# Kernel optimization log

Hardware: AMD Instinct MI355X
Metric: run time of the kernel (lower is better)

Reference implementation:

```python
import jax, jax.numpy as jnp
import numpy as np

B, S, D, F, K = 32, 512, 256, 256, 3

def setup_inputs() -> dict:
    key = jax.random.key(0)
    ks = jax.random.split(key, 8)
    x = jax.random.normal(ks[0], (B, S, D), dtype=jnp.float32)
    target = jax.random.uniform(ks[1], (B, S), dtype=jnp.float32, minval=1.0, maxval=8.0)
    expand_max_len = int(jnp.round(target.sum(-1)).max())
    sc = 0.05
    conv1_w = jax.random.normal(ks[2], (F, D, K), dtype=jnp.float32) * sc
    conv1_b = jnp.zeros((F,), jnp.float32)
    conv2_w = jax.random.normal(ks[3], (F, F, K), dtype=jnp.float32) * sc
    conv2_b = jnp.zeros((F,), jnp.float32)
    norm1_g = jnp.ones((F,), jnp.float32); norm1_b = jnp.zeros((F,), jnp.float32)
    norm2_g = jnp.ones((F,), jnp.float32); norm2_b = jnp.zeros((F,), jnp.float32)
    lin_w = jax.random.normal(ks[4], (F,), dtype=jnp.float32) * sc
    lin_b = jnp.zeros((), jnp.float32)
    return {"x": x, "target": target, "conv1_w": conv1_w, "conv1_b": conv1_b,
            "conv2_w": conv2_w, "conv2_b": conv2_b, "norm1_g": norm1_g, "norm1_b": norm1_b,
            "norm2_g": norm2_g, "norm2_b": norm2_b, "lin_w": lin_w, "lin_b": lin_b,
            "expand_max_len": expand_max_len}

def _layernorm(h, g, b, eps=1e-5):
    mu = jnp.mean(h, axis=-1, keepdims=True)
    var = jnp.mean((h - mu) ** 2, axis=-1, keepdims=True)
    return (h - mu) * jax.lax.rsqrt(var + eps) * g + b

def _conv1d(h_bsd, w, bias):
    # h_bsd: [B,S,C] -> conv over time with 'same' padding -> [B,S,F]
    h = jnp.transpose(h_bsd, (0, 2, 1))  # [B,C,S]
    out = jax.lax.conv_general_dilated(h, w, window_strides=(1,),
                                       padding=[(K // 2, K // 2)],
                                       dimension_numbers=("NCH", "OIH", "NCH"))
    out = out + bias[None, :, None]
    return jnp.transpose(out, (0, 2, 1))  # [B,S,F]

def _duration_predict(x, conv1_w, conv1_b, conv2_w, conv2_b,
                      norm1_g, norm1_b, norm2_g, norm2_b, lin_w, lin_b):
    h = _conv1d(x, conv1_w, conv1_b)
    h = jax.nn.relu(_layernorm(h, norm1_g, norm1_b))  # dropout is identity in eval
    h = _conv1d(h, conv2_w, conv2_b)
    h = jax.nn.relu(_layernorm(h, norm2_g, norm2_b))
    return jax.nn.relu(h @ lin_w + lin_b)  # [B,S]

def _length_regulate(x, target, L):
    d = jnp.round(target)                # [B,S] integer-valued durations
    ends = jnp.cumsum(d, axis=-1)        # [B,S]
    starts = ends - d
    t = jnp.arange(L, dtype=d.dtype)     # [L]
    mask = ((t[None, None, :] >= starts[:, :, None]) &
            (t[None, None, :] < ends[:, :, None])).astype(x.dtype)  # [B,S,L]
    # x^T @ mask -> [B,D,L]; return transposed [B,L,D]
    return jnp.einsum("bsd,bsl->bld", x, mask)

def reference(x, target, conv1_w, conv1_b, conv2_w, conv2_b,
              norm1_g, norm1_b, norm2_g, norm2_b, lin_w, lin_b, expand_max_len):
    predicted_len = _duration_predict(x, conv1_w, conv1_b, conv2_w, conv2_b,
                                      norm1_g, norm1_b, norm2_g, norm2_b, lin_w, lin_b)
    output = _length_regulate(x, target, expand_max_len)
    return (output, predicted_len)
```

## Files before the change

kernel.cpp:

```cpp
#include <hip/hip_runtime.h>
#include <hip/hip_bf16.h>

#define NB 32
#define NS 512
#define NC 256
#define NKSTEP 24
#define ROWS 32
#define HALO_ROWS 34

typedef __attribute__((ext_vector_type(8))) short short8;
typedef __attribute__((ext_vector_type(4))) float f32x4;

__device__ __forceinline__ unsigned pack2(float a, float b) {
    __hip_bfloat16 ha = __float2bfloat16(a), hb = __float2bfloat16(b);
    return ((unsigned)(*(unsigned short*)&hb) << 16) | (unsigned)(*(unsigned short*)&ha);
}

__global__ __launch_bounds__(256) void prep_w2(const float* __restrict__ w1,
                                               const float* __restrict__ w2,
                                               unsigned short* __restrict__ Bp1,
                                               unsigned short* __restrict__ Bp2) {
    const bool second = blockIdx.x >= 256;
    const int f = blockIdx.x & 255, t = threadIdx.x;
    const float* w = second ? w2 : w1;
    unsigned short* Bp = second ? Bp2 : Bp1;
    const float* wf = w + (size_t)f * 768 + t * 3;
    const float v[3] = {wf[0], wf[1], wf[2]};
#pragma unroll
    for (int shift = 0; shift < 3; ++shift) {
        const int k = shift * 256 + t;
        const int o = f * 32 + (k >> 5) * 8192 + (k & 31);
        __hip_bfloat16 h = __float2bfloat16(v[shift]);
        Bp[o] = *(unsigned short*)&h;
    }
}

template <bool FINAL, typename Tin>
__global__ __launch_bounds__(256, 2) void conv_mfma(
    const Tin* __restrict__ in,
    const uint4* __restrict__ Bp,
    const float* __restrict__ bias,
    const float* __restrict__ gamma,
    const float* __restrict__ beta,
    const float* __restrict__ linw,
    const float* __restrict__ linb,
    void* __restrict__ outp)
{
    __shared__ __align__(16) uint4 xs[HALO_ROWS * 32];
    __shared__ float red[ROWS][4][2];
    __shared__ float dotb[ROWS][4];

    const int tid = threadIdx.x;
    const int b   = blockIdx.x >> 4;
    const int s0  = (blockIdx.x & 15) << 5;

    {
        const int slot = tid & 31;
        for (int r = tid >> 5; r < HALO_ROWS; r += 8) {
            const int s = s0 - 1 + r;
            uint4 v = {0u, 0u, 0u, 0u};
            if (s >= 0 && s < NS) {
                if constexpr (sizeof(Tin) == 4) {
                    const float* src = (const float*)in + ((size_t)(b * NS + s)) * NC + slot * 8;
                    const float4 lo = *(const float4*)src;
                    const float4 hi = *(const float4*)(src + 4);
                    v.x = pack2(lo.x, lo.y); v.y = pack2(lo.z, lo.w);
                    v.z = pack2(hi.x, hi.y); v.w = pack2(hi.z, hi.w);
                } else {
                    v = *(const uint4*)((const unsigned short*)in +
                                        ((size_t)(b * NS + s)) * NC + slot * 8);
                }
            }
            xs[r * 32 + (slot ^ ((r & 7) << 2))] = v;
        }
    }
    __syncthreads();

    const int lane = tid & 63;
    const int w    = tid >> 6;
    const int n0   = w << 6;
    const int l15  = lane & 15;
    const int lg   = lane >> 4;

    f32x4 acc[2][4];
#pragma unroll
    for (int mi = 0; mi < 2; ++mi)
#pragma unroll
        for (int ni = 0; ni < 4; ++ni) acc[mi][ni] = (f32x4){0.f, 0.f, 0.f, 0.f};

    const uint4* bbase = Bp + (size_t)(n0 + l15) * 4 + lg;

    auto lda = [&](int ks, int mi) -> short8 {
        const int row  = mi * 16 + l15 + (ks >> 3);
        int slot = ((ks & 7) << 2) + lg;
        slot ^= (row & 7) << 2;
        return *(const short8*)&xs[row * 32 + slot];
    };
    auto ldb = [&](int ks, int ni) -> short8 {
        return *(const short8*)(const void*)(bbase + ks * 1024 + ni * 64);
    };

    short8 areg[2][2], breg[4][4];
#pragma unroll
    for (int q = 0; q < 4; ++q)
#pragma unroll
        for (int ni = 0; ni < 4; ++ni) breg[q][ni] = ldb(q, ni);
#pragma unroll
    for (int p = 0; p < 2; ++p)
#pragma unroll
        for (int mi = 0; mi < 2; ++mi) areg[p][mi] = lda(p, mi);

#pragma unroll
    for (int p = 0; p < NKSTEP; ++p) {
        const int bs = p & 3, as = p & 1;
#pragma unroll
        for (int mi = 0; mi < 2; ++mi)
#pragma unroll
            for (int ni = 0; ni < 4; ++ni)
                acc[mi][ni] = __builtin_amdgcn_mfma_f32_16x16x32_bf16(
                    areg[as][mi], breg[bs][ni], acc[mi][ni], 0, 0, 0);
        if (p + 4 < NKSTEP) {
#pragma unroll
            for (int ni = 0; ni < 4; ++ni) breg[bs][ni] = ldb(p + 4, ni);
        }
        if (p + 2 < NKSTEP) {
#pragma unroll
            for (int mi = 0; mi < 2; ++mi) areg[as][mi] = lda(p + 2, mi);
        }
    }

    float bv[4], gv[4], bt[4], lwv[4];
#pragma unroll
    for (int ni = 0; ni < 4; ++ni) {
        const int col = n0 + ni * 16 + l15;
        bv[ni] = bias[col]; gv[ni] = gamma[col]; bt[ni] = beta[col];
        if constexpr (FINAL) lwv[ni] = linw[col];
    }
#pragma unroll
    for (int mi = 0; mi < 2; ++mi)
#pragma unroll
        for (int ni = 0; ni < 4; ++ni)
#pragma unroll
            for (int i = 0; i < 4; ++i) acc[mi][ni][i] += bv[ni];

#pragma unroll
    for (int mi = 0; mi < 2; ++mi) {
        float s[4] = {0, 0, 0, 0}, q[4] = {0, 0, 0, 0};
#pragma unroll
        for (int ni = 0; ni < 4; ++ni)
#pragma unroll
            for (int i = 0; i < 4; ++i) {
                const float v = acc[mi][ni][i];
                s[i] += v; q[i] += v * v;
            }
#pragma unroll
        for (int i = 0; i < 4; ++i)
#pragma unroll
            for (int m = 1; m < 16; m <<= 1) {
                s[i] += __shfl_xor(s[i], m, 64);
                q[i] += __shfl_xor(q[i], m, 64);
            }
        if (l15 == 0) {
#pragma unroll
            for (int i = 0; i < 4; ++i) {
                red[mi * 16 + lg * 4 + i][w][0] = s[i];
                red[mi * 16 + lg * 4 + i][w][1] = q[i];
            }
        }
    }
    __syncthreads();

#pragma unroll
    for (int mi = 0; mi < 2; ++mi) {
#pragma unroll
        for (int i = 0; i < 4; ++i) {
            const int row = mi * 16 + lg * 4 + i;
            float sum = 0.f, sq = 0.f;
#pragma unroll
            for (int ww = 0; ww < 4; ++ww) { sum += red[row][ww][0]; sq += red[row][ww][1]; }
            const float mu = sum * (1.f / 256.f);
            const float rs = rsqrtf(sq * (1.f / 256.f) - mu * mu + 1e-5f);
            float p = 0.f;
#pragma unroll
            for (int ni = 0; ni < 4; ++ni) {
                const float y = fmaxf(0.f, (acc[mi][ni][i] - mu) * rs * gv[ni] + bt[ni]);
                if constexpr (!FINAL) {
                    __hip_bfloat16 h = __float2bfloat16(y);
                    ((unsigned short*)outp)[((size_t)(b * NS + s0 + row)) * NC +
                                            n0 + ni * 16 + l15] = *(unsigned short*)&h;
                } else {
                    p += y * lwv[ni];
                }
            }
            if constexpr (FINAL) {
#pragma unroll
                for (int m = 1; m < 16; m <<= 1) p += __shfl_xor(p, m, 64);
                if (l15 == 0) dotb[row][w] = p;
            }
        }
    }
    if constexpr (FINAL) {
        __syncthreads();
        if (tid < ROWS) {
            const float tot = dotb[tid][0] + dotb[tid][1] + dotb[tid][2] + dotb[tid][3] + linb[0];
            ((float*)outp)[b * NS + s0 + tid] = fmaxf(0.f, tot);
        }
    }
}

__global__ __launch_bounds__(256) void scan_scatter(const float* __restrict__ target,
                                                    int* __restrict__ idx, int L)
{
    __shared__ int bufa[512], bufb[512];
    const int b = blockIdx.x, t = threadIdx.x;
    const float* tb = target + (size_t)b * NS;
    const int d0 = (int)rintf(tb[t]);
    const int d1 = (int)rintf(tb[t + 256]);
    bufa[t] = d0; bufa[t + 256] = d1;
    __syncthreads();
    int* src = bufa;
    int* dst = bufb;
    for (int off = 1; off < 512; off <<= 1) {
        for (int i = t; i < 512; i += 256) {
            int v = src[i];
            if (i >= off) v += src[i - off];
            dst[i] = v;
        }
        __syncthreads();
        int* tmp = src; src = dst; dst = tmp;
    }
    const int e0 = src[t], e1 = src[t + 256], total = src[511];
    int* ib = idx + (size_t)b * L;
    for (int k = e0 - d0; k < e0; ++k) ib[k] = t;
    for (int k = e1 - d1; k < e1; ++k) ib[k] = t + 256;
    for (int k = total + t; k < L; k += 256) ib[k] = -1;
}

__global__ __launch_bounds__(256) void gather2(const float4* __restrict__ x4,
                                               const int* __restrict__ idx,
                                               float4* __restrict__ out4, int L)
{
    const int b     = blockIdx.y;
    const int frame = blockIdx.x * 4 + (threadIdx.x >> 6);
    const int lane  = threadIdx.x & 63;
    if (frame >= L) return;
    const int pos = idx[(size_t)b * L + frame];
    float4 v = {0.f, 0.f, 0.f, 0.f};
    if (pos >= 0) v = x4[(((size_t)(b * NS + pos)) << 6) + lane];
    out4[(((size_t)b * L + frame) << 6) + lane] = v;
}

extern "C" void kernel_launch(void* const* d_in, const int* in_sizes, int n_in,
                              void* d_out, int out_size, void* d_ws, size_t ws_size,
                              hipStream_t stream)
{
    const float* x    = (const float*)d_in[0];
    const float* targ = (const float*)d_in[1];
    const float* c1w  = (const float*)d_in[2];
    const float* c1b  = (const float*)d_in[3];
    const float* c2w  = (const float*)d_in[4];
    const float* c2b  = (const float*)d_in[5];
    const float* n1g  = (const float*)d_in[6];
    const float* n1b  = (const float*)d_in[7];
    const float* n2g  = (const float*)d_in[8];
    const float* n2b  = (const float*)d_in[9];
    const float* lw   = (const float*)d_in[10];
    const float* lb   = (const float*)d_in[11];

    const int L = (out_size - NB * NS) / (NB * NC);

    unsigned short* Bp1 = (unsigned short*)d_ws;
    unsigned short* Bp2 = Bp1 + 196608;
    unsigned short* h1  = Bp2 + 196608;
    int* idx = (int*)(h1 + (size_t)NB * NS * NC);
    float* out  = (float*)d_out;
    float* pred = out + (size_t)NB * (size_t)L * NC;

    prep_w2<<<dim3(512), 256, 0, stream>>>(c1w, c2w, Bp1, Bp2);

    conv_mfma<false, float><<<dim3(NB * 16), 256, 0, stream>>>(
        x, (const uint4*)Bp1, c1b, n1g, n1b, nullptr, nullptr, (void*)h1);
    conv_mfma<true, unsigned short><<<dim3(NB * 16), 256, 0, stream>>>(
        h1, (const uint4*)Bp2, c2b, n2g, n2b, lw, lb, (void*)pred);

    scan_scatter<<<dim3(NB), 256, 0, stream>>>(targ, idx, L);
    gather2<<<dim3((L + 3) / 4, NB), 256, 0, stream>>>(
        (const float4*)x, idx, (float4*)out, L);
}
```

Baseline: 162.0 us.

## Merge weight prep with duration scan and tune conv prefetch and gather

```diff
diff --git a/kernel.cpp b/kernel.cpp
--- a/kernel.cpp
+++ b/kernel.cpp
@@ -16,27 +16,59 @@
     return ((unsigned)(*(unsigned short*)&hb) << 16) | (unsigned)(*(unsigned short*)&ha);
 }
 
-__global__ __launch_bounds__(256) void prep_w2(const float* __restrict__ w1,
-                                               const float* __restrict__ w2,
-                                               unsigned short* __restrict__ Bp1,
-                                               unsigned short* __restrict__ Bp2) {
-    const bool second = blockIdx.x >= 256;
-    const int f = blockIdx.x & 255, t = threadIdx.x;
-    const float* w = second ? w2 : w1;
-    unsigned short* Bp = second ? Bp2 : Bp1;
-    const float* wf = w + (size_t)f * 768 + t * 3;
-    const float v[3] = {wf[0], wf[1], wf[2]};
-#pragma unroll
-    for (int shift = 0; shift < 3; ++shift) {
-        const int k = shift * 256 + t;
-        const int o = f * 32 + (k >> 5) * 8192 + (k & 31);
-        __hip_bfloat16 h = __float2bfloat16(v[shift]);
-        Bp[o] = *(unsigned short*)&h;
-    }
+__global__ __launch_bounds__(256) void prep_and_scan(
+    const float* __restrict__ w1, const float* __restrict__ w2,
+    unsigned short* __restrict__ Bp1, unsigned short* __restrict__ Bp2,
+    const float* __restrict__ target, int* __restrict__ idx, int L)
+{
+    __shared__ int bufa[512], bufb[512];
+    const int t = threadIdx.x;
+
+    if (blockIdx.x < 512) {
+        const bool second = blockIdx.x >= 256;
+        const int f = blockIdx.x & 255;
+        const float* w = second ? w2 : w1;
+        unsigned short* Bp = second ? Bp2 : Bp1;
+        const float* wf = w + (size_t)f * 768 + t * 3;
+        const float v[3] = {wf[0], wf[1], wf[2]};
+#pragma unroll
+        for (int shift = 0; shift < 3; ++shift) {
+            const int k = shift * 256 + t;
+            const int o = f * 32 + (k >> 5) * 8192 + (k & 31);
+            __hip_bfloat16 h = __float2bfloat16(v[shift]);
+            Bp[o] = *(unsigned short*)&h;
+        }
+        return;
+    }
+
+    const int b = blockIdx.x - 512;
+    const float* tb = target + (size_t)b * NS;
+    const int d0 = (int)rintf(tb[t]);
+    const int d1 = (int)rintf(tb[t + 256]);
+    bufa[t] = d0; bufa[t + 256] = d1;
+    __syncthreads();
+    int* src = bufa;
+    int* dst = bufb;
+    for (int off = 1; off < 512; off <<= 1) {
+        for (int i = t; i < 512; i += 256) {
+            int v = src[i];
+            if (i >= off) v += src[i - off];
+            dst[i] = v;
+        }
+        __syncthreads();
+        int* tmp = src; src = dst; dst = tmp;
+    }
+    const int e0 = src[t], e1 = src[t + 256], total = src[511];
+    int* ib = idx + (size_t)b * L;
+    const int hi0 = e0 < L ? e0 : L;
+    const int hi1 = e1 < L ? e1 : L;
+    for (int k = e0 - d0; k < hi0; ++k) ib[k] = t;
+    for (int k = e1 - d1; k < hi1; ++k) ib[k] = t + 256;
+    for (int k = total + t; k < L; k += 256) ib[k] = -1;
 }
 
 template <bool FINAL, typename Tin>
-__global__ __launch_bounds__(256, 2) void conv_mfma(
+__global__ __launch_bounds__(256, 4) void conv_mfma(
     const Tin* __restrict__ in,
     const uint4* __restrict__ Bp,
     const float* __restrict__ bias,
@@ -100,32 +132,29 @@
         return *(const short8*)(const void*)(bbase + ks * 1024 + ni * 64);
     };
 
-    short8 areg[2][2], breg[4][4];
-#pragma unroll
-    for (int q = 0; q < 4; ++q)
+    short8 areg[2][2], breg[2][4];
+#pragma unroll
+    for (int q = 0; q < 2; ++q) {
 #pragma unroll
         for (int ni = 0; ni < 4; ++ni) breg[q][ni] = ldb(q, ni);
 #pragma unroll
-    for (int p = 0; p < 2; ++p)
-#pragma unroll
-        for (int mi = 0; mi < 2; ++mi) areg[p][mi] = lda(p, mi);
+        for (int mi = 0; mi < 2; ++mi) areg[q][mi] = lda(q, mi);
+    }
 
 #pragma unroll
     for (int p = 0; p < NKSTEP; ++p) {
-        const int bs = p & 3, as = p & 1;
+        const int rs = p & 1;
 #pragma unroll
         for (int mi = 0; mi < 2; ++mi)
 #pragma unroll
             for (int ni = 0; ni < 4; ++ni)
                 acc[mi][ni] = __builtin_amdgcn_mfma_f32_16x16x32_bf16(
-                    areg[as][mi], breg[bs][ni], acc[mi][ni], 0, 0, 0);
-        if (p + 4 < NKSTEP) {
-#pragma unroll
-            for (int ni = 0; ni < 4; ++ni) breg[bs][ni] = ldb(p + 4, ni);
-        }
+                    areg[rs][mi], breg[rs][ni], acc[mi][ni], 0, 0, 0);
         if (p + 2 < NKSTEP) {
 #pragma unroll
-            for (int mi = 0; mi < 2; ++mi) areg[as][mi] = lda(p + 2, mi);
+            for (int ni = 0; ni < 4; ++ni) breg[rs][ni] = ldb(p + 2, ni);
+#pragma unroll
+            for (int mi = 0; mi < 2; ++mi) areg[rs][mi] = lda(p + 2, mi);
         }
     }
 
@@ -208,46 +237,22 @@
     }
 }
 
-__global__ __launch_bounds__(256) void scan_scatter(const float* __restrict__ target,
-                                                    int* __restrict__ idx, int L)
-{
-    __shared__ int bufa[512], bufb[512];
-    const int b = blockIdx.x, t = threadIdx.x;
-    const float* tb = target + (size_t)b * NS;
-    const int d0 = (int)rintf(tb[t]);
-    const int d1 = (int)rintf(tb[t + 256]);
-    bufa[t] = d0; bufa[t + 256] = d1;
-    __syncthreads();
-    int* src = bufa;
-    int* dst = bufb;
-    for (int off = 1; off < 512; off <<= 1) {
-        for (int i = t; i < 512; i += 256) {
-            int v = src[i];
-            if (i >= off) v += src[i - off];
-            dst[i] = v;
-        }
-        __syncthreads();
-        int* tmp = src; src = dst; dst = tmp;
-    }
-    const int e0 = src[t], e1 = src[t + 256], total = src[511];
-    int* ib = idx + (size_t)b * L;
-    for (int k = e0 - d0; k < e0; ++k) ib[k] = t;
-    for (int k = e1 - d1; k < e1; ++k) ib[k] = t + 256;
-    for (int k = total + t; k < L; k += 256) ib[k] = -1;
-}
-
 __global__ __launch_bounds__(256) void gather2(const float4* __restrict__ x4,
                                                const int* __restrict__ idx,
                                                float4* __restrict__ out4, int L)
 {
-    const int b     = blockIdx.y;
-    const int frame = blockIdx.x * 4 + (threadIdx.x >> 6);
-    const int lane  = threadIdx.x & 63;
-    if (frame >= L) return;
-    const int pos = idx[(size_t)b * L + frame];
-    float4 v = {0.f, 0.f, 0.f, 0.f};
-    if (pos >= 0) v = x4[(((size_t)(b * NS + pos)) << 6) + lane];
-    out4[(((size_t)b * L + frame) << 6) + lane] = v;
+    const int b    = blockIdx.y;
+    const int f0   = blockIdx.x * 8 + (threadIdx.x >> 6) * 2;
+    const int lane = threadIdx.x & 63;
+#pragma unroll
+    for (int j = 0; j < 2; ++j) {
+        const int frame = f0 + j;
+        if (frame >= L) return;
+        const int pos = idx[(size_t)b * L + frame];
+        float4 v = {0.f, 0.f, 0.f, 0.f};
+        if (pos >= 0) v = x4[(((size_t)(b * NS + pos)) << 6) + lane];
+        out4[(((size_t)b * L + frame) << 6) + lane] = v;
+    }
 }
 
 extern "C" void kernel_launch(void* const* d_in, const int* in_sizes, int n_in,
@@ -276,14 +281,13 @@
     float* out  = (float*)d_out;
     float* pred = out + (size_t)NB * (size_t)L * NC;
 
-    prep_w2<<<dim3(512), 256, 0, stream>>>(c1w, c2w, Bp1, Bp2);
+    prep_and_scan<<<dim3(512 + NB), 256, 0, stream>>>(c1w, c2w, Bp1, Bp2, targ, idx, L);
 
     conv_mfma<false, float><<<dim3(NB * 16), 256, 0, stream>>>(
         x, (const uint4*)Bp1, c1b, n1g, n1b, nullptr, nullptr, (void*)h1);
     conv_mfma<true, unsigned short><<<dim3(NB * 16), 256, 0, stream>>>(
         h1, (const uint4*)Bp2, c2b, n2g, n2b, lw, lb, (void*)pred);
 
-    scan_scatter<<<dim3(NB), 256, 0, stream>>>(targ, idx, L);
-    gather2<<<dim3((L + 3) / 4, NB), 256, 0, stream>>>(
+    gather2<<<dim3((L + 7) / 8, NB), 256, 0, stream>>>(
         (const float4*)x, idx, (float4*)out, L);
 }
```

New measurement: 158.7 us. 1.02x faster.
